# Kernel optimization log

Measured on AMD Instinct MI355X. Metric: run time of the kernel, lower is better.

## Reference

```python
import jax, jax.numpy as jnp
import numpy as np

B, C, H, W = 128, 3, 256, 256
SHIFT = int(H * 0.125 + 0.5)   # 32, translation ratio=0.125
CS = int(H * 0.5 + 0.5)        # 128, cutout ratio=0.5 (square images)


def setup_inputs() -> dict:
    key = jax.random.key(0)
    k = jax.random.split(key, 8)
    return {
        "imgs": jax.random.uniform(k[0], (B, C, H, W), dtype=jnp.float32),
        "br": jax.random.uniform(k[1], (B, 1, 1, 1), dtype=jnp.float32),
        "sat": jax.random.uniform(k[2], (B, 1, 1, 1), dtype=jnp.float32),
        "con": jax.random.uniform(k[3], (B, 1, 1, 1), dtype=jnp.float32),
        "tx": jax.random.randint(k[4], (B, 1, 1), 0, 2 * SHIFT + 1, dtype=jnp.int32),
        "ty": jax.random.randint(k[5], (B, 1, 1), 0, 2 * SHIFT + 1, dtype=jnp.int32),
        "cx": jax.random.randint(k[6], (B, 1, 1), 0, H + 1, dtype=jnp.int32),
        "cy": jax.random.randint(k[7], (B, 1, 1), 0, W + 1, dtype=jnp.int32),
    }


def _augment(x, br, sat, con, tx, ty, cx, cy):
    # --- color: brightness, saturation, contrast (same order as AUGMENT_FNS['color']) ---
    x = x + (br - 0.5)
    m = x.mean(axis=1, keepdims=True)                 # channel mean
    x = (x - m) * (sat * 2.0) + m
    m = x.mean(axis=(1, 2, 3), keepdims=True)         # per-image mean
    x = (x - m) * (con + 0.5) + m

    # --- translation (ratio=0.125): pad by 1, clamped gather ---
    txs = tx - SHIFT                                   # in [-SHIFT, SHIFT], [B,1,1]
    tys = ty - SHIFT
    gx = jnp.clip(jnp.arange(H, dtype=jnp.int32)[None, :, None] + txs + 1, 0, H + 1)  # [B,H,1]
    gy = jnp.clip(jnp.arange(W, dtype=jnp.int32)[None, None, :] + tys + 1, 0, W + 1)  # [B,1,W]
    x_pad = jnp.pad(x, ((0, 0), (0, 0), (1, 1), (1, 1)))
    bidx = jnp.arange(B)[:, None, None, None]
    cidx = jnp.arange(C)[None, :, None, None]
    x = x_pad[bidx, cidx, gx[:, None, :, :], gy[:, None, :, :]]  # [B,C,H,W]

    # --- cutout (ratio=0.5): zero a CS x CS clamped window per image ---
    grid_x = jnp.clip(jnp.arange(CS, dtype=jnp.int32)[None, :, None] + cx - CS // 2, 0, H - 1)  # [B,CS,1]
    grid_y = jnp.clip(jnp.arange(CS, dtype=jnp.int32)[None, None, :] + cy - CS // 2, 0, W - 1)  # [B,1,CS]
    mask = jnp.ones((B, H, W), x.dtype).at[jnp.arange(B)[:, None, None], grid_x, grid_y].set(0.0)
    return x * mask[:, None, :, :]


def reference(imgs, br, sat, con, tx, ty, cx, cy):
    return _augment(imgs, br, sat, con, tx, ty, cx, cy)
```

## Files before the change

### kernel.cpp

```cpp
#include <hip/hip_runtime.h>

constexpr int BN  = 128;
constexpr int CN  = 3;
constexpr int HN  = 256;
constexpr int WN  = 256;
constexpr int HW  = HN * WN;
constexpr int CHW = CN * HW;
constexpr int SHIFT_ = 32;
constexpr int CS  = 128;
constexpr int RBLK = 8;

typedef float f32x4 __attribute__((ext_vector_type(4)));

__global__ __launch_bounds__(256) void aug_reduce(const float* __restrict__ x,
                                                  float* __restrict__ partial) {
    const int j = blockIdx.x;
    const int b = blockIdx.y;
    const int t = threadIdx.x;
    constexpr int PER_BLOCK = CHW / 4 / RBLK;
    constexpr int ITER = PER_BLOCK / 256;
    const float4* p = reinterpret_cast<const float4*>(x + (size_t)b * CHW)
                      + (size_t)j * PER_BLOCK + t;
    float s0 = 0.f, s1 = 0.f, s2 = 0.f, s3 = 0.f;
    #pragma unroll
    for (int i = 0; i < ITER; i += 4) {
        float4 v0 = p[(i + 0) * 256];
        float4 v1 = p[(i + 1) * 256];
        float4 v2 = p[(i + 2) * 256];
        float4 v3 = p[(i + 3) * 256];
        s0 += (v0.x + v0.y) + (v0.z + v0.w);
        s1 += (v1.x + v1.y) + (v1.z + v1.w);
        s2 += (v2.x + v2.y) + (v2.z + v2.w);
        s3 += (v3.x + v3.y) + (v3.z + v3.w);
    }
    float s = (s0 + s1) + (s2 + s3);
    #pragma unroll
    for (int off = 32; off > 0; off >>= 1) s += __shfl_down(s, off, 64);
    __shared__ float sm[4];
    if ((t & 63) == 0) sm[t >> 6] = s;
    __syncthreads();
    if (t == 0) partial[b * RBLK + j] = (sm[0] + sm[1]) + (sm[2] + sm[3]);
}

__global__ __launch_bounds__(256) void aug_apply(
    const float* __restrict__ x,
    const float* __restrict__ br, const float* __restrict__ sat,
    const float* __restrict__ con,
    const int* __restrict__ tx, const int* __restrict__ ty,
    const int* __restrict__ cx, const int* __restrict__ cy,
    const float* __restrict__ partial, float* __restrict__ out)
{
    const int b  = blockIdx.y;
    const int g  = blockIdx.x * 256 + threadIdx.x;
    const int p0 = g << 2;
    const int h  = p0 >> 8;
    const int w0 = p0 & (WN - 1);

    __shared__ float s_gm;
    if (threadIdx.x == 0) {
        float s = 0.f;
        #pragma unroll
        for (int i = 0; i < RBLK; ++i) s += partial[b * RBLK + i];
        s_gm = s * (1.0f / (float)CHW);
    }
    __syncthreads();
    const float gm = s_gm;

    const float b1 = br[b] - 0.5f;
    const float k  = (con[b] + 0.5f) * (sat[b] * 2.0f);
    const float c2 = con[b] + 0.5f;

    const int sh  = h  + (tx[b] - SHIFT_);
    const int sw0 = w0 + (ty[b] - SHIFT_);
    const int cx0 = cx[b] - CS / 2;
    const int cy0 = cy[b] - CS / 2;
    const int h0 = max(cx0, 0), h1 = min(cx0 + CS - 1, HN - 1);
    const int wc0 = max(cy0, 0), wc1 = min(cy0 + CS - 1, WN - 1);

    const bool rowok   = (sh >= 0) & (sh < HN);
    const bool cut_row = (h >= h0) & (h <= h1);
    const bool cut_all = cut_row & (w0 >= wc0) & (w0 + 3 <= wc1);

    float x0[4], x1[4], x2[4];
    bool  valid[4];

    if (rowok & !cut_all) {
        const float* base = x + (size_t)b * CHW + sh * WN + sw0;
        if (sw0 >= 0 && sw0 + 3 < WN) {
            float4 a, bb, c;
            __builtin_memcpy(&a,  base,          sizeof(float4));
            __builtin_memcpy(&bb, base + HW,     sizeof(float4));
            __builtin_memcpy(&c,  base + 2 * HW, sizeof(float4));
            x0[0]=a.x;  x0[1]=a.y;  x0[2]=a.z;  x0[3]=a.w;
            x1[0]=bb.x; x1[1]=bb.y; x1[2]=bb.z; x1[3]=bb.w;
            x2[0]=c.x;  x2[1]=c.y;  x2[2]=c.z;  x2[3]=c.w;
            #pragma unroll
            for (int i = 0; i < 4; ++i) valid[i] = true;
        } else {
            #pragma unroll
            for (int i = 0; i < 4; ++i) {
                const int sw = sw0 + i;
                const bool ok = (sw >= 0) & (sw < WN);
                valid[i] = ok;
                if (ok) {
                    x0[i] = base[i];
                    x1[i] = base[i + HW];
                    x2[i] = base[i + 2 * HW];
                } else {
                    x0[i] = x1[i] = x2[i] = 0.f;
                }
            }
        }
    } else {
        #pragma unroll
        for (int i = 0; i < 4; ++i) { x0[i]=x1[i]=x2[i]=0.f; valid[i]=false; }
    }

    f32x4 o0, o1, o2;
    #pragma unroll
    for (int i = 0; i < 4; ++i) {
        const int w = w0 + i;
        const bool cut = cut_row & (w >= wc0) & (w <= wc1);
        const bool live = valid[i] & !cut;
        const float cm  = (x0[i] + x1[i] + x2[i]) * (1.0f / 3.0f);
        const float add = c2 * (cm - gm) + gm + b1;
        o0[i] = live ? (k * (x0[i] - cm) + add) : 0.f;
        o1[i] = live ? (k * (x1[i] - cm) + add) : 0.f;
        o2[i] = live ? (k * (x2[i] - cm) + add) : 0.f;
    }

    f32x4* ob = reinterpret_cast<f32x4*>(out + (size_t)b * CHW + p0);
    __builtin_nontemporal_store(o0, ob);
    __builtin_nontemporal_store(o1, ob + HW / 4);
    __builtin_nontemporal_store(o2, ob + 2 * (HW / 4));
}

extern "C" void kernel_launch(void* const* d_in, const int* in_sizes, int n_in,
                              void* d_out, int out_size, void* d_ws, size_t ws_size,
                              hipStream_t stream) {
    const float* imgs = (const float*)d_in[0];
    const float* br   = (const float*)d_in[1];
    const float* sat  = (const float*)d_in[2];
    const float* con  = (const float*)d_in[3];
    const int*   tx   = (const int*)d_in[4];
    const int*   ty   = (const int*)d_in[5];
    const int*   cx   = (const int*)d_in[6];
    const int*   cy   = (const int*)d_in[7];
    float* out = (float*)d_out;
    float* partial = (float*)d_ws;

    aug_reduce<<<dim3(RBLK, BN), 256, 0, stream>>>(imgs, partial);
    aug_apply<<<dim3(HW / 4 / 256, BN), 256, 0, stream>>>(imgs, br, sat, con,
                                                          tx, ty, cx, cy, partial, out);
}
```

Measured before the change: 197.8 us.

## Fuse reduction and apply into one persistent cooperative kernel with grid sync

Replaces the two-kernel reduce-then-apply pipeline with one cooperative persistent kernel. Each block first computes per-slice partial sums, a grid-wide sync follows, and then the same blocks apply the color, translation and cutout transform to the same slices, which keeps data warm in L2/MALL and removes a kernel launch boundary. The cost is a grid barrier, occupancy-sized grids, and the risk that the cooperative launch falls back to the old path. The grid size assumes 256 CUs and is cached in a static variable.

```diff
diff --git a/kernel.cpp b/kernel.cpp
--- a/kernel.cpp
+++ b/kernel.cpp
@@ -1,4 +1,7 @@
 #include <hip/hip_runtime.h>
+#include <hip/hip_cooperative_groups.h>
+
+namespace cg = cooperative_groups;
 
 constexpr int BN  = 128;
 constexpr int CN  = 3;
@@ -8,9 +11,146 @@
 constexpr int CHW = CN * HW;
 constexpr int SHIFT_ = 32;
 constexpr int CS  = 128;
+constexpr int NSLICE = 2048;
+
+typedef float f32x4 __attribute__((ext_vector_type(4)));
+
+__global__ __launch_bounds__(256, 4) void aug_fused(
+    const float* __restrict__ x,
+    const float* __restrict__ br, const float* __restrict__ sat,
+    const float* __restrict__ con,
+    const int* __restrict__ tx, const int* __restrict__ ty,
+    const int* __restrict__ cx, const int* __restrict__ cy,
+    float* __restrict__ ws, float* __restrict__ out)
+{
+    const int t   = threadIdx.x;
+    const int nwg = gridDim.x;
+
+    __shared__ float sm[4];
+    __shared__ float s_gm;
+
+    for (int s = blockIdx.x; s < NSLICE; s += nwg) {
+        const int b = s >> 4;
+        const int j = s & 15;
+        const float4* base = reinterpret_cast<const float4*>(x + (size_t)b * CHW);
+        float a0 = 0.f, a1 = 0.f, a2 = 0.f, a3 = 0.f;
+        #pragma unroll
+        for (int c = 0; c < CN; ++c) {
+            const float4* p = base + c * (HW / 4) + j * 1024 + t;
+            float4 v0 = p[0];
+            float4 v1 = p[256];
+            float4 v2 = p[512];
+            float4 v3 = p[768];
+            a0 += (v0.x + v0.y) + (v0.z + v0.w);
+            a1 += (v1.x + v1.y) + (v1.z + v1.w);
+            a2 += (v2.x + v2.y) + (v2.z + v2.w);
+            a3 += (v3.x + v3.y) + (v3.z + v3.w);
+        }
+        float v = (a0 + a1) + (a2 + a3);
+        #pragma unroll
+        for (int off = 32; off > 0; off >>= 1) v += __shfl_down(v, off, 64);
+        if ((t & 63) == 0) sm[t >> 6] = v;
+        __syncthreads();
+        if (t == 0) ws[s] = (sm[0] + sm[1]) + (sm[2] + sm[3]);
+        __syncthreads();
+    }
+
+    cg::this_grid().sync();
+
+    for (int s = blockIdx.x; s < NSLICE; s += nwg) {
+        const int b = s >> 4;
+        const int j = s & 15;
+
+        if (t == 0) {
+            float g = 0.f;
+            #pragma unroll
+            for (int i = 0; i < 16; ++i) g += ws[b * 16 + i];
+            s_gm = g * (1.0f / (float)CHW);
+        }
+        __syncthreads();
+        const float gm = s_gm;
+
+        const float b1 = br[b] - 0.5f;
+        const float c2 = con[b] + 0.5f;
+        const float k  = c2 * (sat[b] * 2.0f);
+        const int txs  = tx[b] - SHIFT_;
+        const int tys  = ty[b] - SHIFT_;
+        const int cx0  = cx[b] - CS / 2;
+        const int cy0  = cy[b] - CS / 2;
+        const int h0   = max(cx0, 0), h1 = min(cx0 + CS - 1, HN - 1);
+        const int wc0  = max(cy0, 0), wc1 = min(cy0 + CS - 1, WN - 1);
+
+        for (int it = 0; it < 4; ++it) {
+            const int lp = ((it << 8) + t) << 2;
+            const int h  = (j << 4) + (lp >> 8);
+            const int w0 = lp & (WN - 1);
+            const int p0 = (h << 8) + w0;
+
+            const int sh  = h  + txs;
+            const int sw0 = w0 + tys;
+
+            const bool rowok   = (sh >= 0) & (sh < HN);
+            const bool cut_row = (h >= h0) & (h <= h1);
+            const bool cut_all = cut_row & (w0 >= wc0) & (w0 + 3 <= wc1);
+
+            float x0[4], x1[4], x2[4];
+            bool  valid[4];
+
+            if (rowok & !cut_all) {
+                const float* basep = x + (size_t)b * CHW + sh * WN + sw0;
+                if (sw0 >= 0 && sw0 + 3 < WN) {
+                    float4 a, bb, c;
+                    __builtin_memcpy(&a,  basep,          sizeof(float4));
+                    __builtin_memcpy(&bb, basep + HW,     sizeof(float4));
+                    __builtin_memcpy(&c,  basep + 2 * HW, sizeof(float4));
+                    x0[0]=a.x;  x0[1]=a.y;  x0[2]=a.z;  x0[3]=a.w;
+                    x1[0]=bb.x; x1[1]=bb.y; x1[2]=bb.z; x1[3]=bb.w;
+                    x2[0]=c.x;  x2[1]=c.y;  x2[2]=c.z;  x2[3]=c.w;
+                    #pragma unroll
+                    for (int i = 0; i < 4; ++i) valid[i] = true;
+                } else {
+                    #pragma unroll
+                    for (int i = 0; i < 4; ++i) {
+                        const int sw = sw0 + i;
+                        const bool ok = (sw >= 0) & (sw < WN);
+                        valid[i] = ok;
+                        if (ok) {
+                            x0[i] = basep[i];
+                            x1[i] = basep[i + HW];
+                            x2[i] = basep[i + 2 * HW];
+                        } else {
+                            x0[i] = x1[i] = x2[i] = 0.f;
+                        }
+                    }
+                }
+            } else {
+                #pragma unroll
+                for (int i = 0; i < 4; ++i) { x0[i]=x1[i]=x2[i]=0.f; valid[i]=false; }
+            }
+
+            f32x4 o0, o1, o2;
+            #pragma unroll
+            for (int i = 0; i < 4; ++i) {
+                const int w = w0 + i;
+                const bool cut  = cut_row & (w >= wc0) & (w <= wc1);
+                const bool live = valid[i] & !cut;
+                const float cm  = (x0[i] + x1[i] + x2[i]) * (1.0f / 3.0f);
+                const float add = c2 * (cm - gm) + gm + b1;
+                o0[i] = live ? (k * (x0[i] - cm) + add) : 0.f;
+                o1[i] = live ? (k * (x1[i] - cm) + add) : 0.f;
+                o2[i] = live ? (k * (x2[i] - cm) + add) : 0.f;
+            }
+
+            f32x4* ob = reinterpret_cast<f32x4*>(out + (size_t)b * CHW + p0);
+            __builtin_nontemporal_store(o0, ob);
+            __builtin_nontemporal_store(o1, ob + HW / 4);
+            __builtin_nontemporal_store(o2, ob + 2 * (HW / 4));
+        }
+        __syncthreads();
+    }
+}
+
 constexpr int RBLK = 8;
-
-typedef float f32x4 __attribute__((ext_vector_type(4)));
 
 __global__ __launch_bounds__(256) void aug_reduce(const float* __restrict__ x,
                                                   float* __restrict__ partial) {
@@ -147,9 +287,29 @@
     const int*   cx   = (const int*)d_in[6];
     const int*   cy   = (const int*)d_in[7];
     float* out = (float*)d_out;
-    float* partial = (float*)d_ws;
-
-    aug_reduce<<<dim3(RBLK, BN), 256, 0, stream>>>(imgs, partial);
-    aug_apply<<<dim3(HW / 4 / 256, BN), 256, 0, stream>>>(imgs, br, sat, con,
-                                                          tx, ty, cx, cy, partial, out);
+    float* ws  = (float*)d_ws;
+
+    static int s_grid = 0;
+    if (s_grid == 0) {
+        int nb = 0;
+        hipError_t qe = hipOccupancyMaxActiveBlocksPerMultiprocessor(&nb, aug_fused, 256, 0);
+        if (qe != hipSuccess || nb < 1) nb = 1;
+        long g = (long)nb * 256;
+        if (g > NSLICE) g = NSLICE;
+        s_grid = (int)g;
+    }
+
+    void* args[] = {
+        (void*)&imgs, (void*)&br, (void*)&sat, (void*)&con,
+        (void*)&tx, (void*)&ty, (void*)&cx, (void*)&cy,
+        (void*)&ws, (void*)&out
+    };
+    hipError_t err = hipLaunchCooperativeKernel(
+        (const void*)aug_fused, dim3(s_grid), dim3(256), args, 0, stream);
+
+    if (err != hipSuccess) {
+        aug_reduce<<<dim3(RBLK, BN), 256, 0, stream>>>(imgs, ws);
+        aug_apply<<<dim3(HW / 4 / 256, BN), 256, 0, stream>>>(imgs, br, sat, con,
+                                                              tx, ty, cx, cy, ws, out);
+    }
 }
```

Result: slower. 322.8 us (+63.2%).
